# Kernel optimization log

Measured on AMD Instinct MI355X. Metric: run time of the kernel, lower is better.

## Reference

```python
import jax, jax.numpy as jnp
import numpy as np

H = 128          # hidden_size
L = 3            # num_layers
N = 200_000      # total atoms across all fragments
E = 400_000      # bidirectional bonds (avg degree ~2)
G = 8192         # number of molecular subgraphs
ATOM_V = 120
BOND_V = 5


def setup_inputs() -> dict:
    key = jax.random.key(0)
    ks = jax.random.split(key, 14)
    s = 1.0 / np.sqrt(H)
    f = lambda k, shp: (jax.random.normal(k, shp, jnp.float32) * s)
    return {
        "atom_types": jax.random.randint(ks[0], (N,), 0, ATOM_V),
        "edges": jax.random.randint(ks[1], (2, E), 0, N),
        "edge_types": jax.random.randint(ks[2], (E,), 0, BOND_V),
        "node_batch": jnp.sort(jax.random.randint(ks[3], (N,), 0, G)),
        "atom_emb": f(ks[4], (ATOM_V, H)),
        "bond_emb": f(ks[5], (BOND_V, H)),
        "conv_w1": f(ks[6], (L, H, H)),
        "conv_b1": jnp.zeros((L, H), jnp.float32),
        "conv_w2": f(ks[7], (L, H, H)),
        "conv_b2": jnp.zeros((L, H), jnp.float32),
        "proj_w1": f(ks[8], (H, H)),
        "proj_b1": jnp.zeros((H,), jnp.float32),
        "proj_w2": f(ks[9], (H, H)),
        "proj_b2": jnp.zeros((H,), jnp.float32),
    }


def reference(atom_types, edges, edge_types, node_batch,
              atom_emb, bond_emb,
              conv_w1, conv_b1, conv_w2, conv_b2,
              proj_w1, proj_b1, proj_w2, proj_b2):
    # node / bond embeddings (torch clamps indices to vocab-1)
    x = atom_emb[jnp.clip(atom_types, 0, ATOM_V - 1)]       # [N, H]
    a = bond_emb[jnp.clip(edge_types, 0, BOND_V - 1)]       # [E, H]
    src, dst = edges[0], edges[1]
    # GINEConv layers: x_i' = MLP(x_i + sum_{j->i} ReLU(x_j + e_ji)), eps=0
    for l in range(L):
        m = jax.nn.relu(x[src] + a)                         # [E, H] edge messages
        agg = jax.ops.segment_sum(m, dst, num_segments=N)   # scatter-add to dst nodes
        h = x + agg
        h = jax.nn.relu(h @ conv_w1[l] + conv_b1[l])
        x = h @ conv_w2[l] + conv_b2[l]
    # per-graph mean readout
    sums = jax.ops.segment_sum(x, node_batch, num_segments=G)                      # [G, H]
    cnt = jax.ops.segment_sum(jnp.ones((N, 1), x.dtype), node_batch, num_segments=G)
    g = sums / jnp.maximum(cnt, 1.0)
    # proj: Linear -> SiLU -> Linear
    g = jax.nn.silu(g @ proj_w1 + proj_b1)
    return g @ proj_w2 + proj_b2                            # [G, H]
```

## Files before the change

### kernel.cpp

```cpp
#include <hip/hip_runtime.h>

typedef unsigned short u16;
typedef __attribute__((ext_vector_type(8))) short short8;
typedef __attribute__((ext_vector_type(4))) float f32x4;

#define HDIM 128
#define SCAN_B 512

__device__ __forceinline__ float bf2f(u16 v) {
    return __uint_as_float(((unsigned int)v) << 16);
}
__device__ __forceinline__ u16 f2bf(float f) {
    unsigned int u = __float_as_uint(f);
    unsigned int r = (u + 0x7FFFu + ((u >> 16) & 1u)) >> 16;
    return (u16)r;
}

__global__ __launch_bounds__(256) void prep_kernel(
    const float* __restrict__ w1, const float* __restrict__ w2,
    const float* __restrict__ pw1, const float* __restrict__ pw2,
    const float* __restrict__ atom_emb,
    u16* __restrict__ wt, u16* __restrict__ ebf)
{
    int gid = blockIdx.x * 256 + threadIdx.x;
    if (gid < 8 * 16384) {
        int mat = gid >> 14;
        int idx = gid & 16383;
        int n = idx >> 7, k = idx & 127;
        const float* src;
        if      (mat < 3) src = w1 + mat * 16384;
        else if (mat < 6) src = w2 + (mat - 3) * 16384;
        else if (mat == 6) src = pw1;
        else               src = pw2;
        wt[gid] = f2bf(src[k * 128 + n]);
    } else {
        int i = gid - 8 * 16384;
        if (i < 120 * 128) ebf[i] = f2bf(atom_emb[i]);
    }
}

__global__ __launch_bounds__(256) void deg_hist_kernel(
    const int* __restrict__ edges, int* __restrict__ deg, int E, int N)
{
    int e = blockIdx.x * 256 + threadIdx.x;
    if (e >= E) return;
    int d = edges[E + e];
    d = d < 0 ? 0 : (d >= N ? N - 1 : d);
    atomicAdd(&deg[d], 1);
}

__global__ __launch_bounds__(SCAN_B) void scan_block_kernel(
    const int* __restrict__ deg, int* __restrict__ offs, int* __restrict__ bsum, int N)
{
    __shared__ int tmp[SCAN_B];
    int t = threadIdx.x;
    int gid = blockIdx.x * SCAN_B + t;
    int v = (gid < N) ? deg[gid] : 0;
    tmp[t] = v;
    __syncthreads();
#pragma unroll
    for (int off = 1; off < SCAN_B; off <<= 1) {
        int add = (t >= off) ? tmp[t - off] : 0;
        __syncthreads();
        tmp[t] += add;
        __syncthreads();
    }
    if (gid < N) offs[gid] = tmp[t] - v;
    if (t == SCAN_B - 1) bsum[blockIdx.x] = tmp[t];
}

__global__ __launch_bounds__(256) void finalize_offs_kernel(
    int* __restrict__ offs, const int* __restrict__ bsum,
    int* __restrict__ cursor, int N, int E)
{
    __shared__ int red[256];
    const int tid = threadIdx.x;
    const int B = blockIdx.x >> 1;
    int sum = 0;
    for (int t = tid; t < B; t += 256) sum += bsum[t];
    red[tid] = sum;
    __syncthreads();
#pragma unroll
    for (int off = 128; off > 0; off >>= 1) {
        if (tid < off) red[tid] += red[tid + off];
        __syncthreads();
    }
    int prefix = red[0];
    int gid = blockIdx.x * 256 + tid;
    if (gid < N) {
        int v = offs[gid] + prefix;
        offs[gid] = v;
        cursor[gid] = v;
    }
    if (gid == 0) offs[N] = E;
}

__global__ __launch_bounds__(256) void fill_csr_kernel(
    const int* __restrict__ edges, const int* __restrict__ etypes,
    int* __restrict__ cursor, int* __restrict__ csr, int E, int N)
{
    int e = blockIdx.x * 256 + threadIdx.x;
    if (e >= E) return;
    int s = edges[e], d = edges[E + e], t = etypes[e];
    s = s < 0 ? 0 : (s >= N ? N - 1 : s);
    d = d < 0 ? 0 : (d >= N ? N - 1 : d);
    t = t < 0 ? 0 : (t > 4 ? 4 : t);
    int pos = atomicAdd(&cursor[d], 1);
    csr[pos] = (s << 3) | t;
}

__global__ __launch_bounds__(512, 4) void gine_kernel(
    const u16* __restrict__ x_in, u16* __restrict__ x_out,
    const int* __restrict__ types, int use_emb, const u16* __restrict__ ebf,
    const int* __restrict__ offs, const int* __restrict__ csr,
    const float* __restrict__ bond_emb,
    const u16* __restrict__ w1t, const float* __restrict__ b1,
    const u16* __restrict__ w2t, const float* __restrict__ b2, int N)
{
    __shared__ __align__(16) u16 As[128][136];
    __shared__ __align__(16) u16 Ws[128][136];
    __shared__ __align__(16) u16 bsh[5 * 128];
    const int tid  = threadIdx.x;
    const int row0 = blockIdx.x * 128;
    const int wave = tid >> 6, lane = tid & 63;
    const int m = lane & 15, quad = lane >> 4;

    for (int i = tid; i < 640; i += 512) bsh[i] = f2bf(bond_emb[i]);
    {
        const uint4* src = (const uint4*)w1t;
        for (int i = tid; i < 2048; i += 512) {
            int n = i >> 4, k8 = i & 15;
            *(uint4*)&Ws[n][k8 * 8] = src[i];
        }
    }
    {
        const int rp = tid >> 4, c8 = (tid & 15) * 8;
        __syncthreads();

        int rowA = row0 + rp,      rowB = row0 + 32 + rp;
        int rowC = row0 + 64 + rp, rowD = row0 + 96 + rp;
        int rcA = rowA < N ? rowA : N - 1;
        int rcB = rowB < N ? rowB : N - 1;
        int rcC = rowC < N ? rowC : N - 1;
        int rcD = rowD < N ? rowD : N - 1;
        const u16 *spA, *spB, *spC, *spD;
        if (use_emb) {
            int tA = types[rcA]; tA = tA < 0 ? 0 : (tA > 119 ? 119 : tA);
            int tB = types[rcB]; tB = tB < 0 ? 0 : (tB > 119 ? 119 : tB);
            int tC = types[rcC]; tC = tC < 0 ? 0 : (tC > 119 ? 119 : tC);
            int tD = types[rcD]; tD = tD < 0 ? 0 : (tD > 119 ? 119 : tD);
            spA = ebf + (size_t)tA * 128; spB = ebf + (size_t)tB * 128;
            spC = ebf + (size_t)tC * 128; spD = ebf + (size_t)tD * 128;
        } else {
            spA = x_in + (size_t)rcA * 128; spB = x_in + (size_t)rcB * 128;
            spC = x_in + (size_t)rcC * 128; spD = x_in + (size_t)rcD * 128;
        }
        int jbA = offs[rcA], jeA = rowA < N ? offs[rcA + 1] : jbA;
        int jbB = offs[rcB], jeB = rowB < N ? offs[rcB + 1] : jbB;
        int jbC = offs[rcC], jeC = rowC < N ? offs[rcC + 1] : jbC;
        int jbD = offs[rcD], jeD = rowD < N ? offs[rcD + 1] : jbD;
        uint4 svA = *(const uint4*)(spA + c8);
        uint4 svB = *(const uint4*)(spB + c8);
        uint4 svC = *(const uint4*)(spC + c8);
        uint4 svD = *(const uint4*)(spD + c8);
        float accA[8], accB[8], accC[8], accD[8];
        {
            const u16* pA = (const u16*)&svA; const u16* pB = (const u16*)&svB;
            const u16* pC = (const u16*)&svC; const u16* pD = (const u16*)&svD;
#pragma unroll
            for (int i = 0; i < 8; i++) {
                accA[i] = bf2f(pA[i]); accB[i] = bf2f(pB[i]);
                accC[i] = bf2f(pC[i]); accD[i] = bf2f(pD[i]);
            }
        }
        int dA = jeA - jbA, dB = jeB - jbB, dC = jeC - jbC, dD = jeD - jbD;
        int dmax = dA > dB ? dA : dB;
        dmax = dC > dmax ? dC : dmax;
        dmax = dD > dmax ? dD : dmax;
        for (int k = 0; k < dmax; k += 2) {
            bool a0 = k < dA,     a1 = (k + 1) < dA;
            bool a2 = k < dB,     a3 = (k + 1) < dB;
            bool a4 = k < dC,     a5 = (k + 1) < dC;
            bool a6 = k < dD,     a7 = (k + 1) < dD;
            int v0 = a0 ? csr[jbA + k] : 0;  int v1 = a1 ? csr[jbA + k + 1] : 0;
            int v2 = a2 ? csr[jbB + k] : 0;  int v3 = a3 ? csr[jbB + k + 1] : 0;
            int v4 = a4 ? csr[jbC + k] : 0;  int v5 = a5 ? csr[jbC + k + 1] : 0;
            int v6 = a6 ? csr[jbD + k] : 0;  int v7 = a7 ? csr[jbD + k + 1] : 0;
            const u16 *p0, *p1, *p2, *p3, *p4, *p5, *p6, *p7;
            if (use_emb) {
                int t0 = types[v0 >> 3]; t0 = t0 < 0 ? 0 : (t0 > 119 ? 119 : t0);
                int t1 = types[v1 >> 3]; t1 = t1 < 0 ? 0 : (t1 > 119 ? 119 : t1);
                int t2 = types[v2 >> 3]; t2 = t2 < 0 ? 0 : (t2 > 119 ? 119 : t2);
                int t3 = types[v3 >> 3]; t3 = t3 < 0 ? 0 : (t3 > 119 ? 119 : t3);
                int t4 = types[v4 >> 3]; t4 = t4 < 0 ? 0 : (t4 > 119 ? 119 : t4);
                int t5 = types[v5 >> 3]; t5 = t5 < 0 ? 0 : (t5 > 119 ? 119 : t5);
                int t6 = types[v6 >> 3]; t6 = t6 < 0 ? 0 : (t6 > 119 ? 119 : t6);
                int t7 = types[v7 >> 3]; t7 = t7 < 0 ? 0 : (t7 > 119 ? 119 : t7);
                p0 = ebf + (size_t)t0 * 128; p1 = ebf + (size_t)t1 * 128;
                p2 = ebf + (size_t)t2 * 128; p3 = ebf + (size_t)t3 * 128;
                p4 = ebf + (size_t)t4 * 128; p5 = ebf + (size_t)t5 * 128;
                p6 = ebf + (size_t)t6 * 128; p7 = ebf + (size_t)t7 * 128;
            } else {
                p0 = x_in + (size_t)(v0 >> 3) * 128; p1 = x_in + (size_t)(v1 >> 3) * 128;
                p2 = x_in + (size_t)(v2 >> 3) * 128; p3 = x_in + (size_t)(v3 >> 3) * 128;
                p4 = x_in + (size_t)(v4 >> 3) * 128; p5 = x_in + (size_t)(v5 >> 3) * 128;
                p6 = x_in + (size_t)(v6 >> 3) * 128; p7 = x_in + (size_t)(v7 >> 3) * 128;
            }
            uint4 g0 = *(const uint4*)(p0 + c8);
            uint4 g1 = *(const uint4*)(p1 + c8);
            uint4 g2 = *(const uint4*)(p2 + c8);
            uint4 g3 = *(const uint4*)(p3 + c8);
            uint4 g4 = *(const uint4*)(p4 + c8);
            uint4 g5 = *(const uint4*)(p5 + c8);
            uint4 g6 = *(const uint4*)(p6 + c8);
            uint4 g7 = *(const uint4*)(p7 + c8);
            if (a0) { const u16* gp = (const u16*)&g0; const u16* bp = bsh + (v0 & 7) * 128 + c8;
#pragma unroll
                for (int i = 0; i < 8; i++) { float mm = bf2f(gp[i]) + bf2f(bp[i]); accA[i] += mm > 0.f ? mm : 0.f; } }
            if (a1) { const u16* gp = (const u16*)&g1; const u16* bp = bsh + (v1 & 7) * 128 + c8;
#pragma unroll
                for (int i = 0; i < 8; i++) { float mm = bf2f(gp[i]) + bf2f(bp[i]); accA[i] += mm > 0.f ? mm : 0.f; } }
            if (a2) { const u16* gp = (const u16*)&g2; const u16* bp = bsh + (v2 & 7) * 128 + c8;
#pragma unroll
                for (int i = 0; i < 8; i++) { float mm = bf2f(gp[i]) + bf2f(bp[i]); accB[i] += mm > 0.f ? mm : 0.f; } }
            if (a3) { const u16* gp = (const u16*)&g3; const u16* bp = bsh + (v3 & 7) * 128 + c8;
#pragma unroll
                for (int i = 0; i < 8; i++) { float mm = bf2f(gp[i]) + bf2f(bp[i]); accB[i] += mm > 0.f ? mm : 0.f; } }
            if (a4) { const u16* gp = (const u16*)&g4; const u16* bp = bsh + (v4 & 7) * 128 + c8;
#pragma unroll
                for (int i = 0; i < 8; i++) { float mm = bf2f(gp[i]) + bf2f(bp[i]); accC[i] += mm > 0.f ? mm : 0.f; } }
            if (a5) { const u16* gp = (const u16*)&g5; const u16* bp = bsh + (v5 & 7) * 128 + c8;
#pragma unroll
                for (int i = 0; i < 8; i++) { float mm = bf2f(gp[i]) + bf2f(bp[i]); accC[i] += mm > 0.f ? mm : 0.f; } }
            if (a6) { const u16* gp = (const u16*)&g6; const u16* bp = bsh + (v6 & 7) * 128 + c8;
#pragma unroll
                for (int i = 0; i < 8; i++) { float mm = bf2f(gp[i]) + bf2f(bp[i]); accD[i] += mm > 0.f ? mm : 0.f; } }
            if (a7) { const u16* gp = (const u16*)&g7; const u16* bp = bsh + (v7 & 7) * 128 + c8;
#pragma unroll
                for (int i = 0; i < 8; i++) { float mm = bf2f(gp[i]) + bf2f(bp[i]); accD[i] += mm > 0.f ? mm : 0.f; } }
        }
        uint4 ovA = make_uint4(0u,0u,0u,0u), ovB = ovA, ovC = ovA, ovD = ovA;
        if (rowA < N) { u16* op = (u16*)&ovA;
#pragma unroll
            for (int i = 0; i < 8; i++) op[i] = f2bf(accA[i]); }
        if (rowB < N) { u16* op = (u16*)&ovB;
#pragma unroll
            for (int i = 0; i < 8; i++) op[i] = f2bf(accB[i]); }
        if (rowC < N) { u16* op = (u16*)&ovC;
#pragma unroll
            for (int i = 0; i < 8; i++) op[i] = f2bf(accC[i]); }
        if (rowD < N) { u16* op = (u16*)&ovD;
#pragma unroll
            for (int i = 0; i < 8; i++) op[i] = f2bf(accD[i]); }
        *(uint4*)&As[rp][c8]      = ovA;
        *(uint4*)&As[32 + rp][c8] = ovB;
        *(uint4*)&As[64 + rp][c8] = ovC;
        *(uint4*)&As[96 + rp][c8] = ovD;
    }
    __syncthreads();

    f32x4 acc[8];
#pragma unroll
    for (int c = 0; c < 8; c++) acc[c] = (f32x4){0.f, 0.f, 0.f, 0.f};
#pragma unroll
    for (int q = 0; q < 4; q++) {
        short8 a = *(const short8*)&As[wave * 16 + m][q * 32 + quad * 8];
#pragma unroll
        for (int c = 0; c < 8; c++) {
            short8 b = *(const short8*)&Ws[c * 16 + m][q * 32 + quad * 8];
            acc[c] = __builtin_amdgcn_mfma_f32_16x16x32_bf16(a, b, acc[c], 0, 0, 0);
        }
    }
    __syncthreads();
    {
        const uint4* src = (const uint4*)w2t;
        for (int i = tid; i < 2048; i += 512) {
            int n = i >> 4, k8 = i & 15;
            *(uint4*)&Ws[n][k8 * 8] = src[i];
        }
    }
#pragma unroll
    for (int c = 0; c < 8; c++) {
        int col = c * 16 + m;
        float bias = b1[col];
#pragma unroll
        for (int r = 0; r < 4; r++) {
            float v = acc[c][r] + bias;
            v = v > 0.f ? v : 0.f;
            As[wave * 16 + quad * 4 + r][col] = f2bf(v);
        }
    }
    __syncthreads();
    f32x4 acc2[8];
#pragma unroll
    for (int c = 0; c < 8; c++) acc2[c] = (f32x4){0.f, 0.f, 0.f, 0.f};
#pragma unroll
    for (int q = 0; q < 4; q++) {
        short8 a = *(const short8*)&As[wave * 16 + m][q * 32 + quad * 8];
#pragma unroll
        for (int c = 0; c < 8; c++) {
            short8 b = *(const short8*)&Ws[c * 16 + m][q * 32 + quad * 8];
            acc2[c] = __builtin_amdgcn_mfma_f32_16x16x32_bf16(a, b, acc2[c], 0, 0, 0);
        }
    }
    __syncthreads();
#pragma unroll
    for (int c = 0; c < 8; c++) {
        int col = c * 16 + m;
        float bias = b2[col];
#pragma unroll
        for (int r = 0; r < 4; r++)
            As[wave * 16 + quad * 4 + r][col] = f2bf(acc2[c][r] + bias);
    }
    __syncthreads();
    for (int i = tid; i < 2048; i += 512) {
        int r = i >> 4, c8 = (i & 15) * 8;
        int row = row0 + r;
        if (row < N) *(uint4*)(x_out + (size_t)row * 128 + c8) = *(const uint4*)&As[r][c8];
    }
}

__global__ __launch_bounds__(256) void readout_mean_kernel(
    const u16* __restrict__ x, const int* __restrict__ nb,
    u16* __restrict__ gm, int N)
{
    __shared__ int range[2];
    __shared__ float part[16][128];
    int b = blockIdx.x;
    int tid = threadIdx.x;
    if (tid < 2) {
        int target = b + tid;
        int lo = 0, hi = N;
        while (lo < hi) {
            int mid = (lo + hi) >> 1;
            if (nb[mid] < target) lo = mid + 1; else hi = mid;
        }
        range[tid] = lo;
    }
    __syncthreads();
    int s = range[0], e = range[1];
    int rg = tid >> 4, c8 = (tid & 15) * 8;
    float acc[8];
#pragma unroll
    for (int i = 0; i < 8; i++) acc[i] = 0.f;
    for (int n = s + rg; n < e; n += 16) {
        uint4 v = *(const uint4*)(x + (size_t)n * 128 + c8);
        const u16* vp = (const u16*)&v;
#pragma unroll
        for (int i = 0; i < 8; i++) acc[i] += bf2f(vp[i]);
    }
#pragma unroll
    for (int i = 0; i < 8; i++) part[rg][c8 + i] = acc[i];
    __syncthreads();
    if (tid < 128) {
        float sum = 0.f;
#pragma unroll
        for (int g = 0; g < 16; g++) sum += part[g][tid];
        float cnt = (float)((e - s) > 0 ? (e - s) : 1);
        gm[(size_t)b * 128 + tid] = f2bf(sum / cnt);
    }
}

__global__ __launch_bounds__(256) void proj_kernel(
    const u16* __restrict__ gm, float* __restrict__ out,
    const u16* __restrict__ pw1t, const float* __restrict__ pb1,
    const u16* __restrict__ pw2t, const float* __restrict__ pb2, int G)
{
    __shared__ __align__(16) u16 As[64][136];
    __shared__ __align__(16) u16 Ws[128][136];
    const int tid  = threadIdx.x;
    const int row0 = blockIdx.x * 64;
    const int wave = tid >> 6, lane = tid & 63;
    const int m = lane & 15, quad = lane >> 4;

    {
        const uint4* src = (const uint4*)pw1t;
        for (int i = tid; i < 2048; i += 256) {
            int n = i >> 4, k8 = i & 15;
            *(uint4*)&Ws[n][k8 * 8] = src[i];
        }
    }
    for (int i = tid; i < 1024; i += 256) {
        int r = i >> 4, c8 = (i & 15) * 8;
        int row = row0 + r;
        uint4 ov = make_uint4(0u, 0u, 0u, 0u);
        if (row < G) ov = *(const uint4*)(gm + (size_t)row * 128 + c8);
        *(uint4*)&As[r][c8] = ov;
    }
    __syncthreads();
    f32x4 acc[8];
#pragma unroll
    for (int c = 0; c < 8; c++) acc[c] = (f32x4){0.f, 0.f, 0.f, 0.f};
#pragma unroll
    for (int q = 0; q < 4; q++) {
        short8 a = *(const short8*)&As[wave * 16 + m][q * 32 + quad * 8];
#pragma unroll
        for (int c = 0; c < 8; c++) {
            short8 b = *(const short8*)&Ws[c * 16 + m][q * 32 + quad * 8];
            acc[c] = __builtin_amdgcn_mfma_f32_16x16x32_bf16(a, b, acc[c], 0, 0, 0);
        }
    }
    __syncthreads();
    {
        const uint4* src = (const uint4*)pw2t;
        for (int i = tid; i < 2048; i += 256) {
            int n = i >> 4, k8 = i & 15;
            *(uint4*)&Ws[n][k8 * 8] = src[i];
        }
    }
#pragma unroll
    for (int c = 0; c < 8; c++) {
        int col = c * 16 + m;
        float bias = pb1[col];
#pragma unroll
        for (int r = 0; r < 4; r++) {
            float v = acc[c][r] + bias;
            v = v / (1.f + __expf(-v));
            As[wave * 16 + quad * 4 + r][col] = f2bf(v);
        }
    }
    __syncthreads();
    f32x4 acc2[8];
#pragma unroll
    for (int c = 0; c < 8; c++) acc2[c] = (f32x4){0.f, 0.f, 0.f, 0.f};
#pragma unroll
    for (int q = 0; q < 4; q++) {
        short8 a = *(const short8*)&As[wave * 16 + m][q * 32 + quad * 8];
#pragma unroll
        for (int c = 0; c < 8; c++) {
            short8 b = *(const short8*)&Ws[c * 16 + m][q * 32 + quad * 8];
            acc2[c] = __builtin_amdgcn_mfma_f32_16x16x32_bf16(a, b, acc2[c], 0, 0, 0);
        }
    }
#pragma unroll
    for (int c = 0; c < 8; c++) {
        int col = c * 16 + m;
        float bias = pb2[col];
#pragma unroll
        for (int r = 0; r < 4; r++) {
            int row = row0 + wave * 16 + quad * 4 + r;
            if (row < G) out[(size_t)row * 128 + col] = acc2[c][r] + bias;
        }
    }
}

extern "C" void kernel_launch(void* const* d_in, const int* in_sizes, int n_in,
                              void* d_out, int out_size, void* d_ws, size_t ws_size,
                              hipStream_t stream) {
    const int*   atom_types  = (const int*)d_in[0];
    const int*   edges       = (const int*)d_in[1];
    const int*   edge_types  = (const int*)d_in[2];
    const int*   node_batch  = (const int*)d_in[3];
    const float* atom_emb    = (const float*)d_in[4];
    const float* bond_emb    = (const float*)d_in[5];
    const float* conv_w1     = (const float*)d_in[6];
    const float* conv_b1     = (const float*)d_in[7];
    const float* conv_w2     = (const float*)d_in[8];
    const float* conv_b2     = (const float*)d_in[9];
    const float* pw1         = (const float*)d_in[10];
    const float* pb1         = (const float*)d_in[11];
    const float* pw2         = (const float*)d_in[12];
    const float* pb2         = (const float*)d_in[13];
    float* out = (float*)d_out;

    const int N = in_sizes[0];
    const int E = in_sizes[2];
    const int G = out_size / HDIM;
    const int nblk = (N + SCAN_B - 1) / SCAN_B;

    size_t xA_bytes  = (size_t)N * HDIM * sizeof(u16);
    size_t xB_bytes  = (size_t)N * HDIM * sizeof(u16);
    size_t wt_bytes  = (size_t)8 * HDIM * HDIM * sizeof(u16);
    size_t ebf_bytes = (size_t)120 * HDIM * sizeof(u16);
    size_t gm_bytes  = (size_t)G * HDIM * sizeof(u16);
    size_t deg_bytes = (size_t)N * 4;
    size_t off_bytes = (size_t)(N + 1) * 4;
    size_t cur_bytes = (size_t)N * 4;
    size_t bs_bytes  = (size_t)nblk * 4;
    size_t csr_bytes = (size_t)E * 4;
    size_t need = xA_bytes + xB_bytes + wt_bytes + ebf_bytes + gm_bytes +
                  deg_bytes + off_bytes + cur_bytes + bs_bytes + csr_bytes;
    if (ws_size < need) {
        hipMemsetAsync(d_out, 0, (size_t)out_size * sizeof(float), stream);
        return;
    }
    char* p = (char*)d_ws;
    u16* xA   = (u16*)p;  p += xA_bytes;
    u16* xB   = (u16*)p;  p += xB_bytes;
    u16* wt   = (u16*)p;  p += wt_bytes;
    u16* ebf  = (u16*)p;  p += ebf_bytes;
    u16* gm   = (u16*)p;  p += gm_bytes;
    int* deg  = (int*)p;  p += deg_bytes;
    int* offs = (int*)p;  p += off_bytes;
    int* cur  = (int*)p;  p += cur_bytes;
    int* bsum = (int*)p;  p += bs_bytes;
    int* csr  = (int*)p;

    prep_kernel<<<(8 * 16384 + 120 * 128 + 255) / 256, 256, 0, stream>>>(
        conv_w1, conv_w2, pw1, pw2, atom_emb, wt, ebf);

    hipMemsetAsync(deg, 0, deg_bytes, stream);
    deg_hist_kernel<<<(E + 255) / 256, 256, 0, stream>>>(edges, deg, E, N);
    scan_block_kernel<<<nblk, SCAN_B, 0, stream>>>(deg, offs, bsum, N);
    finalize_offs_kernel<<<(N + 255) / 256, 256, 0, stream>>>(offs, bsum, cur, N, E);
    fill_csr_kernel<<<(E + 255) / 256, 256, 0, stream>>>(edges, edge_types, cur, csr, E, N);

    const int gblocks = (N + 127) / 128;
    gine_kernel<<<gblocks, 512, 0, stream>>>(
        xB , xA, atom_types, 1, ebf, offs, csr, bond_emb,
        wt + 0 * 16384, conv_b1 + 0, wt + 3 * 16384, conv_b2 + 0, N);
    gine_kernel<<<gblocks, 512, 0, stream>>>(
        xA, xB, atom_types, 0, ebf, offs, csr, bond_emb,
        wt + 1 * 16384, conv_b1 + 128, wt + 4 * 16384, conv_b2 + 128, N);
    gine_kernel<<<gblocks, 512, 0, stream>>>(
        xB, xA, atom_types, 0, ebf, offs, csr, bond_emb,
        wt + 2 * 16384, conv_b1 + 256, wt + 5 * 16384, conv_b2 + 256, N);

    readout_mean_kernel<<<G, 256, 0, stream>>>(xA, node_batch, gm, N);
    proj_kernel<<<(G + 63) / 64, 256, 0, stream>>>(
        gm, out, wt + 6 * 16384, pb1, wt + 7 * 16384, pb2, G);
}
```

Baseline: 360.0 us.

## Fuse weight prep with degree histogram and stage CSR block in LDS

Merges the weight/embedding bf16 conversion kernel and the degree histogram kernel into one launch, with blocks split by index, to cut one kernel launch. In the GINE kernel, each block cooperatively loads its contiguous CSR edge range (up to 2048 entries) into shared memory, and the neighbour loop reads indices from LDS with a global fallback. This adds 8KB of LDS per block, which may lower occupancy, plus branchy index reads. The staging loop has no barrier after it, but the existing __syncthreads that follows covers it.

```diff
diff --git a/kernel.cpp b/kernel.cpp
--- a/kernel.cpp
+++ b/kernel.cpp
@@ -6,6 +6,8 @@
 
 #define HDIM 128
 #define SCAN_B 512
+#define CSH 2048
+#define PREP_BLOCKS 572
 
 __device__ __forceinline__ float bf2f(u16 v) {
     return __uint_as_float(((unsigned int)v) << 16);
@@ -16,37 +18,36 @@
     return (u16)r;
 }
 
-__global__ __launch_bounds__(256) void prep_kernel(
+__global__ __launch_bounds__(256) void prep_hist_kernel(
     const float* __restrict__ w1, const float* __restrict__ w2,
     const float* __restrict__ pw1, const float* __restrict__ pw2,
     const float* __restrict__ atom_emb,
-    u16* __restrict__ wt, u16* __restrict__ ebf)
-{
-    int gid = blockIdx.x * 256 + threadIdx.x;
-    if (gid < 8 * 16384) {
-        int mat = gid >> 14;
-        int idx = gid & 16383;
-        int n = idx >> 7, k = idx & 127;
-        const float* src;
-        if      (mat < 3) src = w1 + mat * 16384;
-        else if (mat < 6) src = w2 + (mat - 3) * 16384;
-        else if (mat == 6) src = pw1;
-        else               src = pw2;
-        wt[gid] = f2bf(src[k * 128 + n]);
+    u16* __restrict__ wt, u16* __restrict__ ebf,
+    const int* __restrict__ edges, int* __restrict__ deg, int E, int N)
+{
+    if (blockIdx.x < PREP_BLOCKS) {
+        int gid = blockIdx.x * 256 + threadIdx.x;
+        if (gid < 8 * 16384) {
+            int mat = gid >> 14;
+            int idx = gid & 16383;
+            int n = idx >> 7, k = idx & 127;
+            const float* src;
+            if      (mat < 3) src = w1 + mat * 16384;
+            else if (mat < 6) src = w2 + (mat - 3) * 16384;
+            else if (mat == 6) src = pw1;
+            else               src = pw2;
+            wt[gid] = f2bf(src[k * 128 + n]);
+        } else {
+            int i = gid - 8 * 16384;
+            ebf[i] = f2bf(atom_emb[i]);
+        }
     } else {
-        int i = gid - 8 * 16384;
-        if (i < 120 * 128) ebf[i] = f2bf(atom_emb[i]);
-    }
-}
-
-__global__ __launch_bounds__(256) void deg_hist_kernel(
-    const int* __restrict__ edges, int* __restrict__ deg, int E, int N)
-{
-    int e = blockIdx.x * 256 + threadIdx.x;
-    if (e >= E) return;
-    int d = edges[E + e];
-    d = d < 0 ? 0 : (d >= N ? N - 1 : d);
-    atomicAdd(&deg[d], 1);
+        int e = (blockIdx.x - PREP_BLOCKS) * 256 + threadIdx.x;
+        if (e >= E) return;
+        int d = edges[E + e];
+        d = d < 0 ? 0 : (d >= N ? N - 1 : d);
+        atomicAdd(&deg[d], 1);
+    }
 }
 
 __global__ __launch_bounds__(SCAN_B) void scan_block_kernel(
@@ -120,6 +121,7 @@
     __shared__ __align__(16) u16 As[128][136];
     __shared__ __align__(16) u16 Ws[128][136];
     __shared__ __align__(16) u16 bsh[5 * 128];
+    __shared__ __align__(16) int csh[CSH];
     const int tid  = threadIdx.x;
     const int row0 = blockIdx.x * 128;
     const int wave = tid >> 6, lane = tid & 63;
@@ -132,6 +134,13 @@
             int n = i >> 4, k8 = i & 15;
             *(uint4*)&Ws[n][k8 * 8] = src[i];
         }
+    }
+    const int rend = (row0 + 128 < N) ? row0 + 128 : N;
+    const int e0 = offs[row0];
+    {
+        int cnt = offs[rend] - e0;
+        cnt = cnt < CSH ? cnt : CSH;
+        for (int i = tid; i < cnt; i += 512) csh[i] = csr[e0 + i];
     }
     {
         const int rp = tid >> 4, c8 = (tid & 15) * 8;
@@ -173,6 +182,7 @@
                 accC[i] = bf2f(pC[i]); accD[i] = bf2f(pD[i]);
             }
         }
+        int lbA = jbA - e0, lbB = jbB - e0, lbC = jbC - e0, lbD = jbD - e0;
         int dA = jeA - jbA, dB = jeB - jbB, dC = jeC - jbC, dD = jeD - jbD;
         int dmax = dA > dB ? dA : dB;
         dmax = dC > dmax ? dC : dmax;
@@ -182,10 +192,15 @@
             bool a2 = k < dB,     a3 = (k + 1) < dB;
             bool a4 = k < dC,     a5 = (k + 1) < dC;
             bool a6 = k < dD,     a7 = (k + 1) < dD;
-            int v0 = a0 ? csr[jbA + k] : 0;  int v1 = a1 ? csr[jbA + k + 1] : 0;
-            int v2 = a2 ? csr[jbB + k] : 0;  int v3 = a3 ? csr[jbB + k + 1] : 0;
-            int v4 = a4 ? csr[jbC + k] : 0;  int v5 = a5 ? csr[jbC + k + 1] : 0;
-            int v6 = a6 ? csr[jbD + k] : 0;  int v7 = a7 ? csr[jbD + k + 1] : 0;
+            int v0 = 0, v1 = 0, v2 = 0, v3 = 0, v4 = 0, v5 = 0, v6 = 0, v7 = 0;
+            if (a0) { int li = lbA + k;     v0 = (li < CSH) ? csh[li] : csr[jbA + k]; }
+            if (a1) { int li = lbA + k + 1; v1 = (li < CSH) ? csh[li] : csr[jbA + k + 1]; }
+            if (a2) { int li = lbB + k;     v2 = (li < CSH) ? csh[li] : csr[jbB + k]; }
+            if (a3) { int li = lbB + k + 1; v3 = (li < CSH) ? csh[li] : csr[jbB + k + 1]; }
+            if (a4) { int li = lbC + k;     v4 = (li < CSH) ? csh[li] : csr[jbC + k]; }
+            if (a5) { int li = lbC + k + 1; v5 = (li < CSH) ? csh[li] : csr[jbC + k + 1]; }
+            if (a6) { int li = lbD + k;     v6 = (li < CSH) ? csh[li] : csr[jbD + k]; }
+            if (a7) { int li = lbD + k + 1; v7 = (li < CSH) ? csh[li] : csr[jbD + k + 1]; }
             const u16 *p0, *p1, *p2, *p3, *p4, *p5, *p6, *p7;
             if (use_emb) {
                 int t0 = types[v0 >> 3]; t0 = t0 < 0 ? 0 : (t0 > 119 ? 119 : t0);
@@ -496,11 +511,9 @@
     int* bsum = (int*)p;  p += bs_bytes;
     int* csr  = (int*)p;
 
-    prep_kernel<<<(8 * 16384 + 120 * 128 + 255) / 256, 256, 0, stream>>>(
-        conv_w1, conv_w2, pw1, pw2, atom_emb, wt, ebf);
-
     hipMemsetAsync(deg, 0, deg_bytes, stream);
-    deg_hist_kernel<<<(E + 255) / 256, 256, 0, stream>>>(edges, deg, E, N);
+    prep_hist_kernel<<<PREP_BLOCKS + (E + 255) / 256, 256, 0, stream>>>(
+        conv_w1, conv_w2, pw1, pw2, atom_emb, wt, ebf, edges, deg, E, N);
     scan_block_kernel<<<nblk, SCAN_B, 0, stream>>>(deg, offs, bsum, N);
     finalize_offs_kernel<<<(N + 255) / 256, 256, 0, stream>>>(offs, bsum, cur, N, E);
     fill_csr_kernel<<<(E + 255) / 256, 256, 0, stream>>>(edges, edge_types, cur, csr, E, N);
```

After: 361.0 us. Within noise of the previous version (+0.3%).
